# Kernel tuning notes

Measured on AMD Instinct MI355X. Metric: run time of the kernel, lower is better.

Reference implementation:

```python
import jax, jax.numpy as jnp
import numpy as np

BS, SL, N_AGENTS, OBS_DIM, STATE_DIM, N_EDGES, HID = 32, 512, 32, 96, 1024, 64, 256


def _hgcn(w_line, x, H):
    # x: [B, n, 1]; H: [B, n, E]. Faithful to torch HGCN:
    # A = D^{-1/2} H |W| B^{-1} H^T D^{-1/2}, with D, B built from detached H/|W|,
    # inf entries (from 0^{-1} / 0^{-0.5}) zeroed. Diagonal matmuls are implicit scalings.
    w_abs = jnp.abs(w_line)
    Hd = jax.lax.stop_gradient(H)
    d = jnp.einsum('bne,e->bn', Hd, jax.lax.stop_gradient(w_abs))  # [B, n]
    d_is = jnp.where(d > 0, jax.lax.rsqrt(jnp.where(d > 0, d, 1.0)), 0.0)
    b = jnp.sum(Hd, axis=-2)  # [B, E]
    b_inv = jnp.where(b > 0, 1.0 / jnp.where(b > 0, b, 1.0), 0.0)
    t = d_is[..., None] * x                       # D^{-1/2} x
    s = jnp.einsum('bne,bnk->bek', H, t)          # H^T (...)
    s = s * (w_abs[None, :] * b_inv)[..., None]   # |W| B^{-1} (diagonals commute)
    y = jnp.einsum('bne,bek->bnk', H, s)          # H (...)
    return d_is[..., None] * y                    # D^{-1/2} (...)


def _mlp(x, w1, b1, w2, b2):
    return jax.nn.relu(x @ w1 + b1) @ w2 + b2


def setup_inputs() -> dict:
    key = jax.random.key(0)
    ks = jax.random.split(key, 24)
    f = jax.random.normal
    inp = {
        'agent_qs': f(ks[0], (BS, SL, N_AGENTS), jnp.float32),
        'states': f(ks[1], (BS, SL, STATE_DIM), jnp.float32),
        'indiv_us': f(ks[2], (BS, SL, N_AGENTS, OBS_DIM), jnp.float32),
        'edge_W': f(ks[3], (OBS_DIM, N_EDGES), jnp.float32) * 0.1,
        'edge_b': f(ks[4], (N_EDGES,), jnp.float32) * 0.1,
        'wline1': 1.0 + 0.1 * f(ks[5], (N_EDGES,), jnp.float32),
        'wline2': 1.0 + 0.1 * f(ks[6], (N_EDGES,), jnp.float32),
    }
    names = ['hw1', 'hc1', 'hw', 'hc']
    outs = [N_AGENTS, N_AGENTS, N_AGENTS, 1]
    for i, (nm, od) in enumerate(zip(names, outs)):
        inp[nm + '_w1'] = f(ks[7 + 4 * i], (STATE_DIM, HID), jnp.float32) * 0.05
        inp[nm + '_b1'] = f(ks[8 + 4 * i], (HID,), jnp.float32) * 0.05
        inp[nm + '_w2'] = f(ks[9 + 4 * i], (HID, od), jnp.float32) * 0.05
        inp[nm + '_b2'] = f(ks[10 + 4 * i], (od,), jnp.float32) * 0.05
    return inp


def reference(agent_qs, states, indiv_us, edge_W, edge_b, wline1, wline2,
              hw1_w1, hw1_b1, hw1_w2, hw1_b2, hc1_w1, hc1_b1, hc1_w2, hc1_b2,
              hw_w1, hw_b1, hw_w2, hw_b2, hc_w1, hc_b1, hc_w2, hc_b2):
    bs, sl, n = agent_qs.shape
    q = agent_qs.reshape(-1, n)                               # [B, n]
    u = indiv_us.reshape(-1, n, indiv_us.shape[-1])           # [B, n, obs]
    s = states.reshape(-1, states.shape[-1])                  # [B, state_dim]
    H = jax.nn.relu(u @ edge_W + edge_b)                      # hyper_edge_net -> [B, n, E]
    x = q[..., None]                                          # node_features [B, n, 1]
    qs_tot = _hgcn(wline2, _hgcn(wline1, x, H), H)[..., 0]    # two stacked HGCN encoders
    w1 = jnp.abs(_mlp(s, hw1_w1, hw1_b1, hw1_w2, hw1_b2))
    c1 = _mlp(s, hc1_w1, hc1_b1, hc1_w2, hc1_b2)
    qt = jax.nn.elu(qs_tot * w1 + c1)
    w = jnp.abs(_mlp(s, hw_w1, hw_b1, hw_w2, hw_b2))
    c = _mlp(s, hc_w1, hc_b1, hc_w2, hc_b2)[..., 0]
    q_tot = jnp.sum(qt * w, axis=-1) + c
    return q_tot.reshape(bs, sl, 1)
```

## Files before the change

kernel.cpp:

```cpp
#include <hip/hip_runtime.h>
#include <cstdint>

typedef _Float16 f16;
typedef _Float16 f16x2 __attribute__((ext_vector_type(2)));
typedef _Float16 f16x4 __attribute__((ext_vector_type(4)));
typedef _Float16 f16x8 __attribute__((ext_vector_type(8)));
typedef float f32x4 __attribute__((ext_vector_type(4)));

#define AS1U const __attribute__((address_space(1))) unsigned int
#define AS3U __attribute__((address_space(3))) unsigned int

__device__ __forceinline__ void gload_lds16(const void* g, void* l) {
    __builtin_amdgcn_global_load_lds((AS1U*)g, (AS3U*)l, 16, 0, 0);
}

#define WSYNC() asm volatile("s_waitcnt lgkmcnt(0)" ::: "memory")
#define CFENCE() asm volatile("" ::: "memory")

#define BATCH 16384
#define NAG   32
#define OBS   96
#define SDIM  1024
#define NE    64
#define HIDN  256
#define NH    1024

#define NB_HG 4096
#define NB_ST 1024
#define NB_PW 256
#define NB_SM 101
#define NB_MAIN (NB_HG + NB_ST + NB_PW + NB_SM)

__global__ __launch_bounds__(256) void k_main(
    const float* __restrict__ agent_qs, const float* __restrict__ states,
    const float* __restrict__ indiv_us, const float* __restrict__ edge_W,
    const float* __restrict__ edge_b, const float* __restrict__ wline1,
    const float* __restrict__ wline2,
    const float* __restrict__ w1a, const float* __restrict__ w1b,
    const float* __restrict__ w1c, const float* __restrict__ w1d,
    const float* __restrict__ b1a, const float* __restrict__ b1b,
    const float* __restrict__ b1c, const float* __restrict__ b1d,
    const float* __restrict__ w2a, const float* __restrict__ w2b,
    const float* __restrict__ w2c, const float* __restrict__ w2d,
    f16* __restrict__ states16, f16* __restrict__ W1t, float* __restrict__ b1cat,
    f16* __restrict__ W2t, f16* __restrict__ hcw2, float* __restrict__ qs_tot) {
    __shared__ __align__(16) char arena[34304];
    const int tid = threadIdx.x;
    int bid = blockIdx.x;

    if (bid < NB_HG) {
        f16*   eWs   = (f16*)arena;
        float* swa   = (float*)(arena + 13312);
        f16*   HsB   = (f16*)(arena + 13824);
        float* svB   = (float*)(arena + 30720);
        float* sttB  = (float*)(arena + 31744);
        float* sdisB = (float*)(arena + 32256);
        float* sbinvB= (float*)(arena + 33280);

        const int w = tid >> 6, l = tid & 63;
        const int b = bid * 4 + w;
        f16*   Hw    = HsB + w * (32 * 66);
        float* sv    = svB + w * 64;
        float* stt   = sttB + w * 32;
        float* sdis  = sdisB + w * 64;
        float* sbinv = sbinvB + w * 64;

        const int nn = l & 31, half = l >> 5;
        float q = agent_qs[(size_t)b * 32 + nn];

        for (int i = tid; i < 6144; i += 256) {
            int k = i >> 6, n = i & 63;
            eWs[n * 104 + k] = (f16)edge_W[i];
        }
        if (tid < 64) swa[tid] = fabsf(wline1[tid]);
        else if (tid < 128) swa[tid] = fabsf(wline2[tid - 64]);
        __syncthreads();

        const int lm = l & 15, lk = l >> 4;
        const float* ub = indiv_us + (size_t)b * (NAG * OBS);

        #pragma unroll
        for (int mt = 0; mt < 2; mt++) {
            f16x8 af[3];
            #pragma unroll
            for (int ks = 0; ks < 3; ks++) {
                const float* up = ub + (mt * 16 + lm) * 96 + ks * 32 + lk * 8;
                float4 v0 = *(const float4*)up;
                float4 v1 = *(const float4*)(up + 4);
                af[ks] = (f16x8){ (f16)v0.x, (f16)v0.y, (f16)v0.z, (f16)v0.w,
                                  (f16)v1.x, (f16)v1.y, (f16)v1.z, (f16)v1.w };
            }
            #pragma unroll
            for (int nt = 0; nt < 4; nt++) {
                f32x4 acc = {0.f, 0.f, 0.f, 0.f};
                #pragma unroll
                for (int ks = 0; ks < 3; ks++) {
                    f16x8 bb = *(const f16x8*)&eWs[(nt * 16 + lm) * 104 + ks * 32 + lk * 8];
                    acc = __builtin_amdgcn_mfma_f32_16x16x32_f16(af[ks], bb, acc, 0, 0, 0);
                }
                int col = nt * 16 + lm;
                float bias = edge_b[col];
                #pragma unroll
                for (int r = 0; r < 4; r++) {
                    int row = mt * 16 + lk * 4 + r;
                    float hv = acc[r] + bias;
                    Hw[row * 66 + col] = (f16)(hv > 0.f ? hv : 0.f);
                }
            }
        }
        WSYNC();

        float bsum = 0.f;
        #pragma unroll
        for (int n = 0; n < 32; n++) bsum += (float)Hw[n * 66 + l];
        sbinv[l] = bsum > 0.f ? 1.f / bsum : 0.f;

        float dd = 0.f;
        #pragma unroll 8
        for (int e2 = 0; e2 < 32; e2++) {
            f16x2 h2 = *(const f16x2*)&Hw[nn * 66 + e2 * 2];
            dd += (float)h2.x * swa[half * 64 + e2 * 2] + (float)h2.y * swa[half * 64 + e2 * 2 + 1];
        }
        float dis = dd > 0.f ? rsqrtf(dd) : 0.f;
        sdis[l] = dis;
        if (half == 0) stt[nn] = dis * q;
        WSYNC();

        float s1 = 0.f;
        #pragma unroll
        for (int n = 0; n < 32; n++) s1 += (float)Hw[n * 66 + l] * stt[n];
        sv[l] = s1 * swa[l] * sbinv[l];
        WSYNC();

        float y1 = 0.f;
        #pragma unroll 8
        for (int e2 = 0; e2 < 32; e2++) {
            f16x2 h2 = *(const f16x2*)&Hw[nn * 66 + e2 * 2];
            y1 += (float)h2.x * sv[e2 * 2] + (float)h2.y * sv[e2 * 2 + 1];
        }
        float x2 = sdis[nn] * y1;
        if (half == 0) stt[nn] = sdis[32 + nn] * x2;
        WSYNC();

        float s2 = 0.f;
        #pragma unroll
        for (int n = 0; n < 32; n++) s2 += (float)Hw[n * 66 + l] * stt[n];
        sv[l] = s2 * swa[64 + l] * sbinv[l];
        WSYNC();

        float y2 = 0.f;
        #pragma unroll 8
        for (int e2 = 0; e2 < 32; e2++) {
            f16x2 h2 = *(const f16x2*)&Hw[nn * 66 + e2 * 2];
            y2 += (float)h2.x * sv[e2 * 2] + (float)h2.y * sv[e2 * 2 + 1];
        }
        if (half == 0) qs_tot[(size_t)b * 32 + nn] = sdis[32 + nn] * y2;
        return;
    }
    bid -= NB_HG;

    if (bid < NB_ST) {
        int i = bid * 256 + tid;
        const int n4 = BATCH * SDIM / 4;
        const int stride = NB_ST * 256;
        for (; i < n4; i += stride) {
            float4 v = ((const float4*)states)[i];
            f16x4 h = { (f16)v.x, (f16)v.y, (f16)v.z, (f16)v.w };
            ((f16x4*)states16)[i] = h;
        }
        return;
    }
    bid -= NB_ST;
    if (bid < NB_PW) {
        float* tile = (float*)arena;
        int mlp = bid >> 6, rem = bid & 63, kt = rem >> 2, ct = rem & 3;
        const float* src = (mlp == 0) ? w1a : (mlp == 1) ? w1b : (mlp == 2) ? w1c : w1d;
        int k0 = kt * 64, c0 = ct * 64;
        for (int i = tid; i < 4096; i += 256) {
            int kk = i >> 6, cc = i & 63;
            tile[kk * 65 + cc] = src[(size_t)(k0 + kk) * 256 + c0 + cc];
        }
        __syncthreads();
        for (int i = tid; i < 4096; i += 256) {
            int cc = i >> 6, kk = i & 63;
            W1t[(size_t)(mlp * 256 + c0 + cc) * 1024 + k0 + kk] = (f16)tile[kk * 65 + cc];
        }
        return;
    }
    bid -= NB_PW;
    {
        int i = bid * 256 + tid;
        if (i < 24576) {
            int mp = i >> 13, rem = i & 8191, oo = rem >> 8, kk = rem & 255;
            const float* src = (mp == 0) ? w2a : (mp == 1) ? w2b : w2c;
            W2t[i] = (f16)src[kk * 32 + oo];
        } else if (i < 24832) {
            int k = i - 24576;
            hcw2[k] = (f16)w2d[k];
        } else if (i < 25856) {
            int n = i - 24832;
            int mlp = n >> 8, c = n & 255;
            const float* bsrc = (mlp == 0) ? b1a : (mlp == 1) ? b1b : (mlp == 2) ? b1c : b1d;
            b1cat[n] = bsrc[c];
        }
    }
}

__global__ __launch_bounds__(512) void k_gemm(
    const f16* __restrict__ A, const f16* __restrict__ B,
    const float* __restrict__ b1cat, const f16* __restrict__ W2t,
    const f16* __restrict__ hcw2, float* __restrict__ Pp) {
    __shared__ __align__(16) char smem[131072];
    f16* Asb = (f16*)smem;
    f16* Bsb = (f16*)(smem + 65536);
    f16* Ts  = (f16*)smem;

    const int tid = threadIdx.x;
    const int w = tid >> 6, l = tid & 63;
    const int lm = l & 15, lk = l >> 4;
    const int wm = w >> 2, wn = w & 3;
    const int p = blockIdx.x;
    const int xcd = p & 7, s = p >> 3;
    const int mt = xcd * 8 + (s >> 2);
    const int nt = s & 3;
    const int m0 = mt * 256, n0 = nt * 256;
    const int c0 = w * 4;
    const int srow = l >> 3;
    const int gchunk = (l & 7) ^ srow;

    float bj[4];
    #pragma unroll
    for (int j = 0; j < 4; j++) bj[j] = b1cat[n0 + wn * 64 + j * 16 + lm];

    f32x4 acc[8][4];
    #pragma unroll
    for (int i = 0; i < 8; i++)
        #pragma unroll
        for (int j = 0; j < 4; j++) acc[i][j] = (f32x4){0.f, 0.f, 0.f, 0.f};

#define STAGE(KT, BI)                                                                     \
    {                                                                                     \
        f16* Ad = Asb + (BI) * 16384;                                                     \
        f16* Bd = Bsb + (BI) * 16384;                                                     \
        _Pragma("unroll")                                                                 \
        for (int i_ = 0; i_ < 4; i_++) {                                                  \
            int cc = c0 + i_;                                                             \
            gload_lds16(&A[(size_t)(m0 + cc * 8 + srow) * 1024 + (KT) * 64 + gchunk * 8], \
                        &Ad[cc * 512]);                                                   \
            gload_lds16(&B[(size_t)(n0 + cc * 8 + srow) * 1024 + (KT) * 64 + gchunk * 8], \
                        &Bd[cc * 512]);                                                   \
        }                                                                                 \
    }

    STAGE(0, 0);
    STAGE(1, 1);

    for (int kt = 0; kt < 16; kt++) {
        if (kt < 15) { asm volatile("s_waitcnt vmcnt(8)" ::: "memory"); }
        else         { asm volatile("s_waitcnt vmcnt(0)" ::: "memory"); }
        CFENCE(); __builtin_amdgcn_s_barrier(); CFENCE();

        const f16* As_ = Asb + (kt & 1) * 16384;
        const f16* Bs_ = Bsb + (kt & 1) * 16384;
        const int swlo = ((lk ^ (lm & 7)) << 3);
        const int swhi = (((4 + lk) ^ (lm & 7)) << 3);

        f16x8 af[4][2], bf01[2][2], bf23[2][2];

        #pragma unroll
        for (int i = 0; i < 4; i++) {
            af[i][0] = *(const f16x8*)&As_[(wm * 128 + i * 16 + lm) * 64 + swlo];
            af[i][1] = *(const f16x8*)&As_[(wm * 128 + i * 16 + lm) * 64 + swhi];
        }
        #pragma unroll
        for (int j = 0; j < 2; j++) {
            bf01[j][0] = *(const f16x8*)&Bs_[(wn * 64 + j * 16 + lm) * 64 + swlo];
            bf01[j][1] = *(const f16x8*)&Bs_[(wn * 64 + j * 16 + lm) * 64 + swhi];
        }
        __builtin_amdgcn_s_setprio(1);
        #pragma unroll
        for (int ks = 0; ks < 2; ks++)
            #pragma unroll
            for (int i = 0; i < 4; i++)
                #pragma unroll
                for (int j = 0; j < 2; j++)
                    acc[i][j] = __builtin_amdgcn_mfma_f32_16x16x32_f16(af[i][ks], bf01[j][ks], acc[i][j], 0, 0, 0);
        __builtin_amdgcn_s_setprio(0);
        CFENCE(); __builtin_amdgcn_s_barrier(); CFENCE();

        #pragma unroll
        for (int j = 0; j < 2; j++) {
            bf23[j][0] = *(const f16x8*)&Bs_[(wn * 64 + (2 + j) * 16 + lm) * 64 + swlo];
            bf23[j][1] = *(const f16x8*)&Bs_[(wn * 64 + (2 + j) * 16 + lm) * 64 + swhi];
        }
        __builtin_amdgcn_s_setprio(1);
        #pragma unroll
        for (int ks = 0; ks < 2; ks++)
            #pragma unroll
            for (int i = 0; i < 4; i++)
                #pragma unroll
                for (int j = 0; j < 2; j++)
                    acc[i][2 + j] = __builtin_amdgcn_mfma_f32_16x16x32_f16(af[i][ks], bf23[j][ks], acc[i][2 + j], 0, 0, 0);
        __builtin_amdgcn_s_setprio(0);
        CFENCE(); __builtin_amdgcn_s_barrier(); CFENCE();

        #pragma unroll
        for (int i = 0; i < 4; i++) {
            af[i][0] = *(const f16x8*)&As_[(wm * 128 + (4 + i) * 16 + lm) * 64 + swlo];
            af[i][1] = *(const f16x8*)&As_[(wm * 128 + (4 + i) * 16 + lm) * 64 + swhi];
        }
        __builtin_amdgcn_s_setprio(1);
        #pragma unroll
        for (int ks = 0; ks < 2; ks++)
            #pragma unroll
            for (int i = 0; i < 4; i++)
                #pragma unroll
                for (int j = 0; j < 2; j++)
                    acc[4 + i][j] = __builtin_amdgcn_mfma_f32_16x16x32_f16(af[i][ks], bf01[j][ks], acc[4 + i][j], 0, 0, 0);
        __builtin_amdgcn_s_setprio(0);
        CFENCE(); __builtin_amdgcn_s_barrier(); CFENCE();

        if (kt < 14) STAGE(kt + 2, kt & 1);
        __builtin_amdgcn_s_setprio(1);
        #pragma unroll
        for (int ks = 0; ks < 2; ks++)
            #pragma unroll
            for (int i = 0; i < 4; i++)
                #pragma unroll
                for (int j = 0; j < 2; j++)
                    acc[4 + i][2 + j] = __builtin_amdgcn_mfma_f32_16x16x32_f16(af[i][ks], bf23[j][ks], acc[4 + i][2 + j], 0, 0, 0);
        __builtin_amdgcn_s_setprio(0);
    }
#undef STAGE

    __syncthreads();

    const int mlp = nt;
    #pragma unroll
    for (int pass = 0; pass < 2; pass++) {
        if (wm == pass) {
            #pragma unroll
            for (int i = 0; i < 8; i++)
                #pragma unroll
                for (int r = 0; r < 4; r++) {
                    int rl = i * 16 + lk * 4 + r;
                    #pragma unroll
                    for (int j = 0; j < 4; j++) {
                        float v = acc[i][j][r] + bj[j];
                        Ts[rl * 264 + wn * 64 + j * 16 + lm] = (f16)(v > 0.f ? v : 0.f);
                    }
                }
        }
        __syncthreads();
        const int grow = m0 + pass * 128 + w * 16;
        if (mlp < 3) {
            const f16* wb = W2t + mlp * 8192;
            f32x4 acc2[2];
            acc2[0] = (f32x4){0, 0, 0, 0}; acc2[1] = (f32x4){0, 0, 0, 0};
            #pragma unroll
            for (int ks = 0; ks < 8; ks++) {
                f16x8 a  = *(const f16x8*)&Ts[(w * 16 + lm) * 264 + ks * 32 + lk * 8];
                f16x8 b0 = *(const f16x8*)&wb[lm * 256 + ks * 32 + lk * 8];
                f16x8 b1 = *(const f16x8*)&wb[(16 + lm) * 256 + ks * 32 + lk * 8];
                acc2[0] = __builtin_amdgcn_mfma_f32_16x16x32_f16(a, b0, acc2[0], 0, 0, 0);
                acc2[1] = __builtin_amdgcn_mfma_f32_16x16x32_f16(a, b1, acc2[1], 0, 0, 0);
            }
            #pragma unroll
            for (int j2 = 0; j2 < 2; j2++)
                #pragma unroll
                for (int r = 0; r < 4; r++)
                    Pp[(size_t)(grow + lk * 4 + r) * 104 + mlp * 32 + j2 * 16 + lm] = acc2[j2][r];
        } else {
            f32x4 acc2 = (f32x4){0, 0, 0, 0};
            #pragma unroll
            for (int ks = 0; ks < 8; ks++) {
                f16x8 a = *(const f16x8*)&Ts[(w * 16 + lm) * 264 + ks * 32 + lk * 8];
                f16x8 bz = (f16x8){0, 0, 0, 0, 0, 0, 0, 0};
                if (lm == 0) bz = *(const f16x8*)&hcw2[ks * 32 + lk * 8];
                acc2 = __builtin_amdgcn_mfma_f32_16x16x32_f16(a, bz, acc2, 0, 0, 0);
            }
            if (lm == 0)
                #pragma unroll
                for (int r = 0; r < 4; r++)
                    Pp[(size_t)(grow + lk * 4 + r) * 104 + 96] = acc2[r];
        }
        if (pass == 0) __syncthreads();
    }
}

__global__ __launch_bounds__(256) void k_ep(
    const float* __restrict__ Pp, const float* __restrict__ qs_tot,
    const float* __restrict__ hw1_b2, const float* __restrict__ hc1_b2,
    const float* __restrict__ hw_b2, const float* __restrict__ hc_b2,
    float* __restrict__ out) {
    const int tid = threadIdx.x;
    const int row = blockIdx.x * 32 + (tid >> 3);
    const int q8 = tid & 7, o = q8 * 4;
    const float* p0 = Pp + (size_t)row * 104;
    f32x4 a0 = *(const f32x4*)(p0 + o);
    f32x4 c0 = *(const f32x4*)(p0 + 32 + o);
    f32x4 w0 = *(const f32x4*)(p0 + 64 + o);
    f32x4 qs = *(const f32x4*)(qs_tot + (size_t)row * 32 + o);
    float val = 0.f;
    #pragma unroll
    for (int j = 0; j < 4; j++) {
        float wv1 = fabsf(a0[j] + hw1_b2[o + j]);
        float cv1 = c0[j] + hc1_b2[o + j];
        float wv  = fabsf(w0[j] + hw_b2[o + j]);
        float z = qs[j] * wv1 + cv1;
        float qt = z > 0.f ? z : expm1f(z);
        val += qt * wv;
    }
    val += __shfl_xor(val, 1);
    val += __shfl_xor(val, 2);
    val += __shfl_xor(val, 4);
    if (q8 == 0) out[row] = val + p0[96] + hc_b2[0];
}

extern "C" void kernel_launch(void* const* d_in, const int* in_sizes, int n_in,
                              void* d_out, int out_size, void* d_ws, size_t ws_size,
                              hipStream_t stream) {
    const float* agent_qs = (const float*)d_in[0];
    const float* states   = (const float*)d_in[1];
    const float* indiv_us = (const float*)d_in[2];
    const float* edge_W   = (const float*)d_in[3];
    const float* edge_b   = (const float*)d_in[4];
    const float* wline1   = (const float*)d_in[5];
    const float* wline2   = (const float*)d_in[6];
    const float* hw1_w1 = (const float*)d_in[7];
    const float* hw1_b1 = (const float*)d_in[8];
    const float* hw1_w2 = (const float*)d_in[9];
    const float* hw1_b2 = (const float*)d_in[10];
    const float* hc1_w1 = (const float*)d_in[11];
    const float* hc1_b1 = (const float*)d_in[12];
    const float* hc1_w2 = (const float*)d_in[13];
    const float* hc1_b2 = (const float*)d_in[14];
    const float* hw_w1  = (const float*)d_in[15];
    const float* hw_b1  = (const float*)d_in[16];
    const float* hw_w2  = (const float*)d_in[17];
    const float* hw_b2  = (const float*)d_in[18];
    const float* hc_w1  = (const float*)d_in[19];
    const float* hc_b1  = (const float*)d_in[20];
    const float* hc_w2  = (const float*)d_in[21];
    const float* hc_b2  = (const float*)d_in[22];

    char* ws = (char*)d_ws;
    size_t o_states16 = 0;
    size_t o_W1t  = o_states16 + (size_t)BATCH * SDIM * 2;
    size_t o_b1   = o_W1t + (size_t)NH * SDIM * 2;
    size_t o_W2t  = o_b1 + 4096;
    size_t o_hcw2 = o_W2t + 49152;
    size_t o_Pp   = o_hcw2 + 512;
    size_t o_qs   = o_Pp + (size_t)BATCH * 104 * 4;

    f16*   states16 = (f16*)(ws + o_states16);
    f16*   W1t      = (f16*)(ws + o_W1t);
    float* b1cat    = (float*)(ws + o_b1);
    f16*   W2t      = (f16*)(ws + o_W2t);
    f16*   hcw2     = (f16*)(ws + o_hcw2);
    float* Pp       = (float*)(ws + o_Pp);
    float* qs_tot   = (float*)(ws + o_qs);

    k_main<<<NB_MAIN, 256, 0, stream>>>(
        agent_qs, states, indiv_us, edge_W, edge_b, wline1, wline2,
        hw1_w1, hc1_w1, hw_w1, hc_w1, hw1_b1, hc1_b1, hw_b1, hc_b1,
        hw1_w2, hc1_w2, hw_w2, hc_w2,
        states16, W1t, b1cat, W2t, hcw2, qs_tot);
    k_gemm<<<256, 512, 0, stream>>>(states16, W1t, b1cat, W2t, hcw2, Pp);
    k_ep<<<BATCH / 32, 256, 0, stream>>>(Pp, qs_tot, hw1_b2, hc1_b2, hw_b2, hc_b2,
                                         (float*)d_out);
}
```

Before: 115.5 us.

## Interleave state-conversion blocks with HGCN blocks and keep per-lane scalars in registers

The 4096 HGCN blocks and 1024 states fp32-to-fp16 conversion blocks are merged into one 5120-block range, with every fifth block doing conversion. Bandwidth-bound conversion work then overlaps with the compute-heavy HGCN blocks instead of running in a separate phase. The sdis and sbinv LDS arrays are replaced by registers, using a cross-half shuffle for the degree scalings, and |W| is cached per lane. This shrinks shared memory, and launch_bounds now requests 5 blocks per CU, which may limit registers and cause spills.

```diff
diff --git a/kernel.cpp b/kernel.cpp
--- a/kernel.cpp
+++ b/kernel.cpp
@@ -25,13 +25,12 @@
 #define HIDN  256
 #define NH    1024
 
-#define NB_HG 4096
-#define NB_ST 1024
-#define NB_PW 256
-#define NB_SM 101
-#define NB_MAIN (NB_HG + NB_ST + NB_PW + NB_SM)
-
-__global__ __launch_bounds__(256) void k_main(
+#define NB_MIX 5120
+#define NB_PW  256
+#define NB_SM  101
+#define NB_MAIN (NB_MIX + NB_PW + NB_SM)
+
+__global__ __launch_bounds__(256, 5) void k_main(
     const float* __restrict__ agent_qs, const float* __restrict__ states,
     const float* __restrict__ indiv_us, const float* __restrict__ edge_W,
     const float* __restrict__ edge_b, const float* __restrict__ wline1,
@@ -44,26 +43,35 @@
     const float* __restrict__ w2c, const float* __restrict__ w2d,
     f16* __restrict__ states16, f16* __restrict__ W1t, float* __restrict__ b1cat,
     f16* __restrict__ W2t, f16* __restrict__ hcw2, float* __restrict__ qs_tot) {
-    __shared__ __align__(16) char arena[34304];
+    __shared__ __align__(16) char arena[32256];
     const int tid = threadIdx.x;
     int bid = blockIdx.x;
 
-    if (bid < NB_HG) {
-        f16*   eWs   = (f16*)arena;
-        float* swa   = (float*)(arena + 13312);
-        f16*   HsB   = (f16*)(arena + 13824);
-        float* svB   = (float*)(arena + 30720);
-        float* sttB  = (float*)(arena + 31744);
-        float* sdisB = (float*)(arena + 32256);
-        float* sbinvB= (float*)(arena + 33280);
+    if (bid < NB_MIX) {
+        const int g = bid / 5, r = bid - g * 5;
+        if (r == 4) {
+            int i = g * 256 + tid;
+            const int n4 = BATCH * SDIM / 4;
+            const int stride = 1024 * 256;
+            for (; i < n4; i += stride) {
+                float4 v = ((const float4*)states)[i];
+                f16x4 h = { (f16)v.x, (f16)v.y, (f16)v.z, (f16)v.w };
+                ((f16x4*)states16)[i] = h;
+            }
+            return;
+        }
+        const int hbid = g * 4 + r;
+        f16*   eWs  = (f16*)arena;
+        float* swa  = (float*)(arena + 13312);
+        f16*   HsB  = (f16*)(arena + 13824);
+        float* svB  = (float*)(arena + 30720);
+        float* sttB = (float*)(arena + 31744);
 
         const int w = tid >> 6, l = tid & 63;
-        const int b = bid * 4 + w;
-        f16*   Hw    = HsB + w * (32 * 66);
-        float* sv    = svB + w * 64;
-        float* stt   = sttB + w * 32;
-        float* sdis  = sdisB + w * 64;
-        float* sbinv = sbinvB + w * 64;
+        const int b = hbid * 4 + w;
+        f16*   Hw  = HsB + w * (32 * 66);
+        float* sv  = svB + w * 64;
+        float* stt = sttB + w * 32;
 
         const int nn = l & 31, half = l >> 5;
         float q = agent_qs[(size_t)b * 32 + nn];
@@ -75,6 +83,9 @@
         if (tid < 64) swa[tid] = fabsf(wline1[tid]);
         else if (tid < 128) swa[tid] = fabsf(wline2[tid - 64]);
         __syncthreads();
+
+        const float swal1 = swa[l];
+        const float swal2 = swa[64 + l];
 
         const int lm = l & 15, lk = l >> 4;
         const float* ub = indiv_us + (size_t)b * (NAG * OBS);
@@ -101,9 +112,9 @@
                 int col = nt * 16 + lm;
                 float bias = edge_b[col];
                 #pragma unroll
-                for (int r = 0; r < 4; r++) {
-                    int row = mt * 16 + lk * 4 + r;
-                    float hv = acc[r] + bias;
+                for (int r2 = 0; r2 < 4; r2++) {
+                    int row = mt * 16 + lk * 4 + r2;
+                    float hv = acc[r2] + bias;
                     Hw[row * 66 + col] = (f16)(hv > 0.f ? hv : 0.f);
                 }
             }
@@ -113,7 +124,7 @@
         float bsum = 0.f;
         #pragma unroll
         for (int n = 0; n < 32; n++) bsum += (float)Hw[n * 66 + l];
-        sbinv[l] = bsum > 0.f ? 1.f / bsum : 0.f;
+        const float sbinv_r = bsum > 0.f ? 1.f / bsum : 0.f;
 
         float dd = 0.f;
         #pragma unroll 8
@@ -122,14 +133,16 @@
             dd += (float)h2.x * swa[half * 64 + e2 * 2] + (float)h2.y * swa[half * 64 + e2 * 2 + 1];
         }
         float dis = dd > 0.f ? rsqrtf(dd) : 0.f;
-        sdis[l] = dis;
+        const float dis_o = __shfl_xor(dis, 32);
+        const float dis1 = (half == 0) ? dis : dis_o;
+        const float dis2 = (half == 0) ? dis_o : dis;
         if (half == 0) stt[nn] = dis * q;
         WSYNC();
 
         float s1 = 0.f;
         #pragma unroll
         for (int n = 0; n < 32; n++) s1 += (float)Hw[n * 66 + l] * stt[n];
-        sv[l] = s1 * swa[l] * sbinv[l];
+        sv[l] = s1 * swal1 * sbinv_r;
         WSYNC();
 
         float y1 = 0.f;
@@ -138,14 +151,14 @@
             f16x2 h2 = *(const f16x2*)&Hw[nn * 66 + e2 * 2];
             y1 += (float)h2.x * sv[e2 * 2] + (float)h2.y * sv[e2 * 2 + 1];
         }
-        float x2 = sdis[nn] * y1;
-        if (half == 0) stt[nn] = sdis[32 + nn] * x2;
+        float x2 = dis1 * y1;
+        if (half == 0) stt[nn] = dis2 * x2;
         WSYNC();
 
         float s2 = 0.f;
         #pragma unroll
         for (int n = 0; n < 32; n++) s2 += (float)Hw[n * 66 + l] * stt[n];
-        sv[l] = s2 * swa[64 + l] * sbinv[l];
+        sv[l] = s2 * swal2 * sbinv_r;
         WSYNC();
 
         float y2 = 0.f;
@@ -154,23 +167,11 @@
             f16x2 h2 = *(const f16x2*)&Hw[nn * 66 + e2 * 2];
             y2 += (float)h2.x * sv[e2 * 2] + (float)h2.y * sv[e2 * 2 + 1];
         }
-        if (half == 0) qs_tot[(size_t)b * 32 + nn] = sdis[32 + nn] * y2;
+        if (half == 0) qs_tot[(size_t)b * 32 + nn] = dis2 * y2;
         return;
     }
-    bid -= NB_HG;
-
-    if (bid < NB_ST) {
-        int i = bid * 256 + tid;
-        const int n4 = BATCH * SDIM / 4;
-        const int stride = NB_ST * 256;
-        for (; i < n4; i += stride) {
-            float4 v = ((const float4*)states)[i];
-            f16x4 h = { (f16)v.x, (f16)v.y, (f16)v.z, (f16)v.w };
-            ((f16x4*)states16)[i] = h;
-        }
-        return;
-    }
-    bid -= NB_ST;
+    bid -= NB_MIX;
+
     if (bid < NB_PW) {
         float* tile = (float*)arena;
         int mlp = bid >> 6, rem = bid & 63, kt = rem >> 2, ct = rem & 3;
```

After: 116.6 us (median of 2 runs). No clear change (+1.0%).
